# Kernel optimization log

Hardware: AMD Instinct MI355X
Metric: run time of the kernel (lower is better)

The kernel has to match this reference:

```python
import jax, jax.numpy as jnp
import numpy as np

# Static graph-batch geometry (equal-size graphs -> uniform per-graph k, jit-friendly)
B = 512        # number of graphs
N_PER = 2048   # nodes per graph
C = 64         # in_channels
DEG = 16       # average degree
K = 1024       # ceil(ratio * N_PER) with ratio = 0.5
N = B * N_PER
E = B * N_PER * DEG


def setup_inputs() -> dict:
    key = jax.random.key(0)
    k1, k2, k3 = jax.random.split(key, 3)
    x = jax.random.normal(k1, (N, C), dtype=jnp.float32)
    # edges are intra-graph: local endpoints in [0, N_PER) plus per-graph node offset
    local = jax.random.randint(k2, (2, E), 0, N_PER, dtype=jnp.int32)
    offs = jnp.repeat(jnp.arange(B, dtype=jnp.int32) * N_PER, N_PER * DEG)
    edge_index = local + offs[None, :]
    batch = jnp.repeat(jnp.arange(B, dtype=jnp.int32), N_PER)
    p = jax.random.normal(k3, (C,), dtype=jnp.float32)  # SelectTopK projection weight
    return {"x": x, "edge_index": edge_index, "batch": batch, "p": p}


def reference(x, edge_index, batch, p):
    # SelectTopK: y = tanh(x @ p / ||p||), per-graph top-k
    y = jnp.tanh(x @ p / jnp.linalg.norm(p))            # [N]
    scores, local_idx = jax.lax.top_k(y.reshape(B, N_PER), K)   # [B, K] each
    perm = (local_idx.astype(jnp.int32)
            + jnp.arange(B, dtype=jnp.int32)[:, None] * N_PER).reshape(-1)  # [B*K] global ids
    score = scores.reshape(-1)                          # [B*K]
    # gather + scale (multiplier == 1)
    x_out = x[perm] * score[:, None]                    # [B*K, C]
    # FilterEdges / connect: remap kept nodes to new contiguous ids, mask dropped edges
    node_map = jnp.full((N,), -1, dtype=jnp.int32).at[perm].set(
        jnp.arange(B * K, dtype=jnp.int32))
    new_src = node_map[edge_index[0]]
    new_dst = node_map[edge_index[1]]
    edge_mask = (new_src >= 0) & (new_dst >= 0)         # [E] which edges survive
    new_edge_index = jnp.where(edge_mask[None, :],
                               jnp.stack([new_src, new_dst]), -1)  # dropped edges = -1
    new_batch = batch[perm]
    return x_out, new_edge_index, new_batch, perm, score
```

## Files before the change

### kernel.cpp

```cpp
#include <hip/hip_runtime.h>
#include <cstdint>
#include <cstddef>

#define NB 512
#define N_PER 2048
#define NC 64
#define DEG 16
#define KSEL 1024
#define NTOT (NB * N_PER)
#define ETOT (NTOT * DEG)
#define NOUT (NB * KSEL)

#define T 1024
#define EPT 2


__global__ __launch_bounds__(T, 8) void fused_topk_kernel(
    const float* __restrict__ x, const float* __restrict__ p,
    const int* __restrict__ ei,
    float* __restrict__ out_x, float* __restrict__ out_edge,
    float* __restrict__ out_batch, float* __restrict__ out_perm,
    float* __restrict__ out_score) {
  __shared__ unsigned long long key2[EPT][T];
  __shared__ int lmap[N_PER];
  __shared__ int klist[KSEL];
  __shared__ float kscore[KSEL];
  __shared__ double p_s[NC];
  __shared__ double norm_s;

  const int tid = threadIdx.x;
  const int b = blockIdx.x;
  const int base = b * N_PER;

  if (tid < NC) p_s[tid] = (double)p[tid];
  __syncthreads();
  if (tid == 0) {
    double s = 0.0;
    for (int i = 0; i < NC; ++i) s += p_s[i] * p_s[i];
    norm_s = sqrt(s);
  }

  const int lane = tid & 15;
  const int rowg = tid >> 4;
  const double pw0 = p_s[lane * 4 + 0];
  const double pw1 = p_s[lane * 4 + 1];
  const double pw2 = p_s[lane * 4 + 2];
  const double pw3 = p_s[lane * 4 + 3];
  const float4* xrow = (const float4*)(x + (size_t)base * NC);

  for (int r0 = 0; r0 < N_PER; r0 += 64) {
    const int row = r0 + rowg;
    float4 v = xrow[row * 16 + lane];
    double part = (double)v.x * pw0 + (double)v.y * pw1 +
                  (double)v.z * pw2 + (double)v.w * pw3;
    part += __shfl_xor(part, 8, 16);
    part += __shfl_xor(part, 4, 16);
    part += __shfl_xor(part, 2, 16);
    part += __shfl_xor(part, 1, 16);
    if (lane == 0) {
      unsigned long long u = (unsigned long long)__double_as_longlong(part);
      unsigned long long asc =
          (u & 0x8000000000000000ULL) ? ~u : (u | 0x8000000000000000ULL);
      unsigned long long desc = ~asc;
      key2[row & 1][row >> 1] = (desc & ~2047ULL) | (unsigned long long)row;
    }
  }
  __syncthreads();

  unsigned long long r0k = key2[0][tid];
  unsigned long long r1k = key2[1][tid];

  auto CE = [](unsigned long long& a, unsigned long long& c, bool up) {
    if ((a > c) == up) { unsigned long long t = a; a = c; c = t; }
  };
  auto shfl_stage = [&](int m, bool up) {
    const bool keepmin = (((tid & m) == 0) == up);
    unsigned long long o0 = __shfl_xor(r0k, m, 64);
    unsigned long long o1 = __shfl_xor(r1k, m, 64);
    if (keepmin ? (o0 < r0k) : (o0 > r0k)) r0k = o0;
    if (keepmin ? (o1 < r1k) : (o1 > r1k)) r1k = o1;
  };
  auto lds_stage = [&](int m, bool up) {
    __syncthreads();
    key2[0][tid] = r0k;
    key2[1][tid] = r1k;
    __syncthreads();
    const bool keepmin = (((tid & m) == 0) == up);
    unsigned long long o0 = key2[0][tid ^ m];
    unsigned long long o1 = key2[1][tid ^ m];
    if (keepmin ? (o0 < r0k) : (o0 > r0k)) r0k = o0;
    if (keepmin ? (o1 < r1k) : (o1 > r1k)) r1k = o1;
  };

  CE(r0k, r1k, (tid & 1) == 0);
#pragma unroll
  for (int k = 4; k <= N_PER; k <<= 1) {
    const bool up = ((tid & (k >> 1)) == 0);
#pragma unroll
    for (int j = (k >> 1); j >= 128; j >>= 1) lds_stage(j >> 1, up);
#pragma unroll
    for (int j = ((k >> 1) > 64 ? 64 : (k >> 1)); j >= 2; j >>= 1)
      shfl_stage(j >> 1, up);
    CE(r0k, r1k, up);
  }

  __syncthreads();
  const double norm = norm_s;
#pragma unroll
  for (int s = 0; s < EPT; ++s) {
    const unsigned long long key = (s == 0) ? r0k : r1k;
    const int pos = tid * EPT + s;
    const int idx = (int)(key & 2047ULL);
    if (pos < KSEL) {
      unsigned long long desc = key & ~2047ULL;
      unsigned long long asc = ~desc;
      unsigned long long u = (asc & 0x8000000000000000ULL)
                                 ? (asc ^ 0x8000000000000000ULL)
                                 : ~asc;
      const double dot = __longlong_as_double((long long)u);
      const float sc = tanhf((float)(dot / norm));
      const int nid = b * KSEL + pos;
      out_batch[nid] = (float)b;
      out_perm[nid] = (float)(base + idx);
      out_score[nid] = sc;
      klist[pos] = idx;
      kscore[pos] = sc;
      lmap[idx] = nid;
    } else {
      lmap[idx] = -1;
    }
  }
  __syncthreads();

  const float4* xg = (const float4*)x;
  float4* xo = (float4*)out_x;
#pragma unroll 4
  for (int rr = 0; rr < KSEL; rr += 64) {
    const int row = rr + rowg;
    const int idx = klist[row];
    const float sc = kscore[row];
    float4 v = xg[(size_t)(base + idx) * 16 + lane];
    v.x *= sc; v.y *= sc; v.z *= sc; v.w *= sc;
    xo[(size_t)(b * KSEL + row) * 16 + lane] = v;
  }

  const int nE4 = N_PER * DEG / 4;
  const int4* s_ei = (const int4*)ei + (size_t)b * nE4;
  const int4* d_ei = (const int4*)(ei + (size_t)ETOT) + (size_t)b * nE4;
  float4* o_s = (float4*)out_edge + (size_t)b * nE4;
  float4* o_d = (float4*)(out_edge + (size_t)ETOT) + (size_t)b * nE4;
#pragma unroll 2
  for (int i = tid; i < nE4; i += T) {
    const int4 s4 = s_ei[i];
    const int4 d4 = d_ei[i];
    const int ns0 = lmap[s4.x - base], ns1 = lmap[s4.y - base];
    const int ns2 = lmap[s4.z - base], ns3 = lmap[s4.w - base];
    const int nd0 = lmap[d4.x - base], nd1 = lmap[d4.y - base];
    const int nd2 = lmap[d4.z - base], nd3 = lmap[d4.w - base];
    float4 os, od;
    const bool k0 = (ns0 >= 0) && (nd0 >= 0);
    const bool k1 = (ns1 >= 0) && (nd1 >= 0);
    const bool k2 = (ns2 >= 0) && (nd2 >= 0);
    const bool k3 = (ns3 >= 0) && (nd3 >= 0);
    os.x = k0 ? (float)ns0 : -1.0f; od.x = k0 ? (float)nd0 : -1.0f;
    os.y = k1 ? (float)ns1 : -1.0f; od.y = k1 ? (float)nd1 : -1.0f;
    os.z = k2 ? (float)ns2 : -1.0f; od.z = k2 ? (float)nd2 : -1.0f;
    os.w = k3 ? (float)ns3 : -1.0f; od.w = k3 ? (float)nd3 : -1.0f;
    o_s[i] = os;
    o_d[i] = od;
  }
}

extern "C" void kernel_launch(void* const* d_in, const int* in_sizes, int n_in,
                              void* d_out, int out_size, void* d_ws,
                              size_t ws_size, hipStream_t stream) {
  const float* x = (const float*)d_in[0];
  const int* ei = (const int*)d_in[1];
  const float* p = (const float*)d_in[3];

  float* out = (float*)d_out;
  float* out_x = out;
  float* out_edge = out + 33554432;
  float* out_batch = out + 67108864;
  float* out_perm = out + 67633152;
  float* out_score = out + 68157440;

  fused_topk_kernel<<<NB, T, 0, stream>>>(x, p, ei, out_x, out_edge, out_batch,
                                          out_perm, out_score);
}
```

Measured before the change: 576.7 us.

## Fuse bitonic LDS stage pairs and truncate final merge to top half

Restructures the in-block bitonic sort so two LDS compare-exchange stages are done per barrier pair, reading three partner keys, which cuts the number of __syncthreads. The final merge only fully sorts the lower half needed for top-k, and upper-half threads stop after the first split. Compare-exchange uses branchless selects. This adds extra LDS reads per fused stage and more complex control flow.

Measured after the change: 574.3 us. No clear change (-0.4%).

```diff
diff --git a/kernel.cpp b/kernel.cpp
--- a/kernel.cpp
+++ b/kernel.cpp
@@ -70,41 +70,118 @@
   unsigned long long r0k = key2[0][tid];
   unsigned long long r1k = key2[1][tid];
 
+  auto SEL = [](unsigned long long a, unsigned long long c, bool keepmin) {
+    return keepmin ? (a < c ? a : c) : (a > c ? a : c);
+  };
   auto CE = [](unsigned long long& a, unsigned long long& c, bool up) {
     if ((a > c) == up) { unsigned long long t = a; a = c; c = t; }
   };
   auto shfl_stage = [&](int m, bool up) {
-    const bool keepmin = (((tid & m) == 0) == up);
+    const bool km = (((tid & m) == 0) == up);
     unsigned long long o0 = __shfl_xor(r0k, m, 64);
     unsigned long long o1 = __shfl_xor(r1k, m, 64);
-    if (keepmin ? (o0 < r0k) : (o0 > r0k)) r0k = o0;
-    if (keepmin ? (o1 < r1k) : (o1 > r1k)) r1k = o1;
-  };
-  auto lds_stage = [&](int m, bool up) {
-    __syncthreads();
-    key2[0][tid] = r0k;
-    key2[1][tid] = r1k;
-    __syncthreads();
-    const bool keepmin = (((tid & m) == 0) == up);
-    unsigned long long o0 = key2[0][tid ^ m];
-    unsigned long long o1 = key2[1][tid ^ m];
-    if (keepmin ? (o0 < r0k) : (o0 > r0k)) r0k = o0;
-    if (keepmin ? (o1 < r1k) : (o1 > r1k)) r1k = o1;
+    r0k = SEL(r0k, o0, km);
+    r1k = SEL(r1k, o1, km);
+  };
+  auto shfl_tail = [&](bool up) {
+    shfl_stage(32, up); shfl_stage(16, up); shfl_stage(8, up);
+    shfl_stage(4, up);  shfl_stage(2, up);  shfl_stage(1, up);
+    CE(r0k, r1k, up);
+  };
+  auto lds_single = [&](int m, bool up) {
+    __syncthreads();
+    key2[0][tid] = r0k; key2[1][tid] = r1k;
+    __syncthreads();
+    const bool km = (((tid & m) == 0) == up);
+    r0k = SEL(r0k, key2[0][tid ^ m], km);
+    r1k = SEL(r1k, key2[1][tid ^ m], km);
+  };
+  auto lds_pair = [&](int m, int m2, bool up) {
+    __syncthreads();
+    key2[0][tid] = r0k; key2[1][tid] = r1k;
+    __syncthreads();
+    const bool kmJ = (((tid & m) == 0) == up);
+    const bool kmJ2 = (((tid & m2) == 0) == up);
+    {
+      unsigned long long pj = key2[0][tid ^ m];
+      unsigned long long pj2 = key2[0][tid ^ m2];
+      unsigned long long pjj = key2[0][tid ^ m ^ m2];
+      r0k = SEL(SEL(r0k, pj, kmJ), SEL(pj2, pjj, kmJ), kmJ2);
+    }
+    {
+      unsigned long long pj = key2[1][tid ^ m];
+      unsigned long long pj2 = key2[1][tid ^ m2];
+      unsigned long long pjj = key2[1][tid ^ m ^ m2];
+      r1k = SEL(SEL(r1k, pj, kmJ), SEL(pj2, pjj, kmJ), kmJ2);
+    }
   };
 
   CE(r0k, r1k, (tid & 1) == 0);
 #pragma unroll
-  for (int k = 4; k <= N_PER; k <<= 1) {
+  for (int k = 4; k <= 128; k <<= 1) {
     const bool up = ((tid & (k >> 1)) == 0);
 #pragma unroll
-    for (int j = (k >> 1); j >= 128; j >>= 1) lds_stage(j >> 1, up);
-#pragma unroll
-    for (int j = ((k >> 1) > 64 ? 64 : (k >> 1)); j >= 2; j >>= 1)
-      shfl_stage(j >> 1, up);
+    for (int j = (k >> 1); j >= 2; j >>= 1) shfl_stage(j >> 1, up);
     CE(r0k, r1k, up);
   }
-
-  __syncthreads();
+  {
+    const bool up = ((tid & 128) == 0);
+    lds_single(64, up);
+    shfl_tail(up);
+  }
+  {
+    const bool up = ((tid & 256) == 0);
+    lds_pair(128, 64, up);
+    shfl_tail(up);
+  }
+  {
+    const bool up = ((tid & 512) == 0);
+    lds_pair(256, 128, up);
+    lds_single(64, up);
+    shfl_tail(up);
+  }
+  __syncthreads();
+  key2[0][tid] = r0k; key2[1][tid] = r1k;
+  __syncthreads();
+  if (tid < 512) {
+    const bool kmJ2 = ((tid & 256) == 0);
+    {
+      unsigned long long pj = key2[0][tid ^ 512];
+      unsigned long long pj2 = key2[0][tid ^ 256];
+      unsigned long long pjj = key2[0][tid ^ 768];
+      r0k = SEL(SEL(r0k, pj, true), SEL(pj2, pjj, true), kmJ2);
+    }
+    {
+      unsigned long long pj = key2[1][tid ^ 512];
+      unsigned long long pj2 = key2[1][tid ^ 256];
+      unsigned long long pjj = key2[1][tid ^ 768];
+      r1k = SEL(SEL(r1k, pj, true), SEL(pj2, pjj, true), kmJ2);
+    }
+  } else {
+    r0k = SEL(r0k, key2[0][tid ^ 512], false);
+    r1k = SEL(r1k, key2[1][tid ^ 512], false);
+  }
+  __syncthreads();
+  if (tid < 512) { key2[0][tid] = r0k; key2[1][tid] = r1k; }
+  __syncthreads();
+  if (tid < 512) {
+    const bool kmJ = ((tid & 128) == 0);
+    const bool kmJ2 = ((tid & 64) == 0);
+    {
+      unsigned long long pj = key2[0][tid ^ 128];
+      unsigned long long pj2 = key2[0][tid ^ 64];
+      unsigned long long pjj = key2[0][tid ^ 192];
+      r0k = SEL(SEL(r0k, pj, kmJ), SEL(pj2, pjj, kmJ), kmJ2);
+    }
+    {
+      unsigned long long pj = key2[1][tid ^ 128];
+      unsigned long long pj2 = key2[1][tid ^ 64];
+      unsigned long long pjj = key2[1][tid ^ 192];
+      r1k = SEL(SEL(r1k, pj, kmJ), SEL(pj2, pjj, kmJ), kmJ2);
+    }
+    shfl_tail(true);
+  }
+
   const double norm = norm_s;
 #pragma unroll
   for (int s = 0; s < EPT; ++s) {
```
